# Kernel tuning notes

Measured on AMD Instinct MI355X. Metric: run time of the kernel, lower is better.

## Reference

```python
import jax, jax.numpy as jnp
import numpy as np

N = 100000     # nodes
E = 1600000    # edges (avg degree 16)
CI = 3         # input features (x, z, t)
W = 128        # hidden width
CO = 1         # output features
L = 4          # processor layers


def setup_inputs() -> dict:
    key = jax.random.key(0)
    ks = jax.random.split(key, 10)
    s = 0.1
    x = jax.random.normal(ks[0], (N, CI), jnp.float32)
    # compute_mask is an external geometry-dependent, no-grad mask; emulate as 0/1 node mask
    mask = (jax.random.uniform(ks[1], (N, 1)) > 0.5).astype(jnp.float32)
    edge_index = jax.random.randint(ks[2], (2, E), 0, N, dtype=jnp.int32)
    W_enc = jax.random.normal(ks[3], (CI, W), jnp.float32) * s
    b_enc = jnp.zeros((W,), jnp.float32)
    W_p = jax.random.normal(ks[4], (L, W, W), jnp.float32) * s
    b_p = jnp.zeros((L, W), jnp.float32)
    W_dec = jax.random.normal(ks[5], (W, CO), jnp.float32) * s
    b_dec = jnp.zeros((CO,), jnp.float32)
    return {"x": x, "mask": mask, "edge_index": edge_index,
            "W_enc": W_enc, "b_enc": b_enc, "W_p": W_p, "b_p": b_p,
            "W_dec": W_dec, "b_dec": b_dec}


def reference(x, mask, edge_index, W_enc, b_enc, W_p, b_p, W_dec, b_dec):
    src, dst = edge_index[0], edge_index[1]
    n = x.shape[0]
    # GCN symmetric normalization with self-loops: deg = 1 + in-degree
    deg = 1.0 + jax.ops.segment_sum(jnp.ones((src.shape[0],), x.dtype), dst, num_segments=n)
    dis = jax.lax.rsqrt(deg)                      # deg^{-1/2}, [N]
    norm = dis[src] * dis[dst]                    # [E]

    def gcn(h, Wt, b):
        h = h @ Wt                                # [N, out]
        agg = jax.ops.segment_sum(h[src] * norm[:, None], dst, num_segments=n)
        # self-loop contribution: norm_ii = dis_i^2
        return agg + h * (dis * dis)[:, None] + b

    h = jax.nn.relu(gcn(x, W_enc, b_enc))
    for l in range(L):
        h = jax.nn.relu(gcn(h, W_p[l], b_p[l]))
    out = gcn(h, W_dec, b_dec)
    return out * mask
```

## Files before the change

### kernel.cpp

```cpp
#include <hip/hip_runtime.h>
#include <hip/hip_fp16.h>


#define HW 128
#define NBMAX 1024
#define CAP 4096
#define PBLK 256

typedef _Float16 f16x8 __attribute__((ext_vector_type(8)));
typedef float f32x4 __attribute__((ext_vector_type(4)));

__global__ void k_zero_i32(int* __restrict__ a, int n) {
    int i = blockIdx.x * 256 + threadIdx.x;
    if (i < n) a[i] = 0;
}

__global__ __launch_bounds__(256) void k_histb(const int* __restrict__ dstA,
                                               int* __restrict__ bcnt,
                                               int* __restrict__ pcnt,
                                               int nb, int e, int nblk) {
    __shared__ int lh[NBMAX];
    for (int b = threadIdx.x; b < nb; b += 256) lh[b] = 0;
    __syncthreads();
    int blk = blockIdx.x;
    int c0 = (int)(((long long)e * blk) / nblk);
    int c1 = (int)(((long long)e * (blk + 1)) / nblk);
    for (int i = c0 + threadIdx.x; i < c1; i += 256) atomicAdd(&lh[dstA[i] >> 7], 1);
    __syncthreads();
    for (int b = threadIdx.x; b < nb; b += 256) {
        int v = lh[b];
        pcnt[(size_t)blk * nb + b] = v;
        if (v) atomicAdd(&bcnt[b], v);
    }
}

__global__ void k_bscan(const int* __restrict__ bcnt, int* __restrict__ bstart,
                        int nb, int etot) {
    __shared__ int s[1024];
    int t = threadIdx.x;
    int d0 = (t < nb) ? bcnt[t] : 0;
    s[t] = d0;
    __syncthreads();
    for (int off = 1; off < 1024; off <<= 1) {
        int v = (t >= off) ? s[t - off] : 0;
        __syncthreads();
        s[t] += v;
        __syncthreads();
    }
    if (t < nb) bstart[t] = s[t] - d0;
    if (t == 0) bstart[nb] = etot;
}

__global__ __launch_bounds__(PBLK) void k_soff2(const int* __restrict__ pcnt,
                                                const int* __restrict__ bstart,
                                                int* __restrict__ soff, int nb) {
    __shared__ int s[PBLK];
    int b = blockIdx.x, t = threadIdx.x;
    int v = pcnt[(size_t)t * nb + b];
    s[t] = v;
    __syncthreads();
    for (int off = 1; off < PBLK; off <<= 1) {
        int u = (t >= off) ? s[t - off] : 0;
        __syncthreads();
        s[t] += u;
        __syncthreads();
    }
    soff[(size_t)t * nb + b] = bstart[b] + s[t] - v;
}

__global__ __launch_bounds__(256) void k_part(const int* __restrict__ srcA,
                                              const int* __restrict__ dstA,
                                              const int* __restrict__ soff,
                                              unsigned* __restrict__ stage,
                                              int nb, int e, int nblk) {
    __shared__ int loff[NBMAX];
    __shared__ int lh[NBMAX];
    int blk = blockIdx.x;
    for (int b = threadIdx.x; b < nb; b += 256) {
        loff[b] = soff[(size_t)blk * nb + b];
        lh[b] = 0;
    }
    __syncthreads();
    int c0 = (int)(((long long)e * blk) / nblk);
    int c1 = (int)(((long long)e * (blk + 1)) / nblk);
    for (int i = c0 + threadIdx.x; i < c1; i += 256) {
        int d = dstA[i];
        int bk = d >> 7;
        int p = loff[bk] + atomicAdd(&lh[bk], 1);
        stage[p] = ((unsigned)srcA[i] << 7) | (unsigned)(d & 127);
    }
}

__global__ __launch_bounds__(256) void k_build(const unsigned* __restrict__ stage,
                                               const int* __restrict__ bstart,
                                               const float* __restrict__ x,
                                               int* __restrict__ row_start,
                                               float* __restrict__ dis,
                                               float4* __restrict__ x4,
                                               int* __restrict__ csr, int n, int nb) {
    __shared__ int lcnt[128];
    __shared__ int sc[128];
    __shared__ int lcsr[CAP];
    int b = blockIdx.x, tid = threadIdx.x;
    int base = bstart[b], end = bstart[b + 1], cnt = end - base;
    int node0 = b << 7;

    if (tid < 128) lcnt[tid] = 0;
    __syncthreads();
    for (int j = tid; j < cnt; j += 256) atomicAdd(&lcnt[stage[base + j] & 127], 1);
    __syncthreads();
    if (tid < 128) sc[tid] = lcnt[tid];
    __syncthreads();
    for (int off = 1; off < 128; off <<= 1) {
        int v = (tid < 128 && tid >= off) ? sc[tid - off] : 0;
        __syncthreads();
        if (tid < 128) sc[tid] += v;
        __syncthreads();
    }
    int node = node0 + tid;
    if (tid < 128 && node < n) {
        int excl = sc[tid] - lcnt[tid];
        row_start[node] = base + excl;
        float dv = rsqrtf(1.f + (float)lcnt[tid]);
        dis[node] = dv;
        x4[node] = make_float4(x[node * 3] * dv, x[node * 3 + 1] * dv,
                               x[node * 3 + 2] * dv, 0.f);
    }
    if (tid == 0 && b == nb - 1) row_start[n] = end;
    __syncthreads();
    if (tid < 128) sc[tid] = sc[tid] - lcnt[tid];
    if (tid < 128) lcnt[tid] = 0;
    __syncthreads();
    if (cnt <= CAP) {
        for (int j = tid; j < cnt; j += 256) {
            unsigned v = stage[base + j];
            int dl = v & 127;
            int p = atomicAdd(&lcnt[dl], 1);
            lcsr[sc[dl] + p] = (int)(v >> 7);
        }
        __syncthreads();
        for (int j = tid; j < cnt; j += 256) csr[base + j] = lcsr[j];
    } else {
        for (int j = tid; j < cnt; j += 256) {
            unsigned v = stage[base + j];
            int dl = v & 127;
            int p = atomicAdd(&lcnt[dl], 1);
            csr[base + sc[dl] + p] = (int)(v >> 7);
        }
    }
}

__global__ void k_prep_wt(const float* __restrict__ Wp, __half* __restrict__ WTh,
                          __half* __restrict__ WTl, int total) {
    int t = blockIdx.x * 256 + threadIdx.x;
    if (t >= total) return;
    int l = t >> 14;
    int kc = t & 16383;
    int k = kc >> 7, c = kc & 127;
    float w = Wp[t];
    __half hi = __float2half_rn(w);
    __half lo = __float2half_rn(w - __half2float(hi));
    size_t o = ((size_t)l << 14) + (size_t)c * HW + k;
    WTh[o] = hi;
    WTl[o] = lo;
}

__global__ void k_enc_agg(const float4* __restrict__ x4, const int* __restrict__ rs,
                          const int* __restrict__ csr, const float* __restrict__ dis,
                          float4* __restrict__ zx, int n) {
    int i = blockIdx.x * 256 + threadIdx.x;
    if (i >= n) return;
    float4 a = x4[i];
    int e1 = rs[i + 1];
    for (int j = rs[i]; j < e1; ++j) {
        float4 v = x4[csr[j]];
        a.x += v.x; a.y += v.y; a.z += v.z;
    }
    float d = dis[i];
    zx[i] = make_float4(a.x * d, a.y * d, a.z * d, 0.f);
}

__global__ void k_enc_gemm(const float4* __restrict__ zx, const float* __restrict__ We,
                           const float* __restrict__ be, const float* __restrict__ dis,
                           __half* __restrict__ H, int n) {
    int t = blockIdx.x * 256 + threadIdx.x;
    int i = t >> 7;
    int c = t & 127;
    if (i >= n) return;
    float4 z = zx[i];
    float v = z.x * We[c] + z.y * We[HW + c] + z.z * We[2 * HW + c] + be[c];
    H[(size_t)i * HW + c] = __float2half_rn(fmaxf(v, 0.f) * dis[i]);
}

__global__ __launch_bounds__(256) void k_agg128(const __half* __restrict__ Hin,
                                                const int* __restrict__ rs,
                                                const int* __restrict__ csr,
                                                const float* __restrict__ dis,
                                                __half* __restrict__ Z, int n) {
    int wave = threadIdx.x >> 6, lane = threadIdx.x & 63;
    int lg = lane & 15;
    int node = (blockIdx.x * 4 + wave) * 4 + (lane >> 4);
    bool active = node < n;

    float a0[8], a1[8], a2[8], a3[8];
#pragma unroll
    for (int j = 0; j < 8; ++j) { a0[j] = 0.f; a1[j] = 0.f; a2[j] = 0.f; a3[j] = 0.f; }

    int e0 = 0, e1 = 0;
    if (active) {
        e0 = rs[node];
        e1 = rs[node + 1];
        f16x8 hv = *(const f16x8*)(Hin + (size_t)node * HW + lg * 8);
#pragma unroll
        for (int j = 0; j < 8; ++j) a0[j] = (float)hv[j];
    }

    for (int base = e0; base < e1; base += 16) {
        int cnt = e1 - base;
        if (cnt > 16) cnt = 16;
        int sl = (base + lg < e1) ? csr[base + lg] : 0;
        int k = 0;
        for (; k + 4 <= cnt; k += 4) {
            int s0 = __shfl(sl, k + 0, 16);
            int s1 = __shfl(sl, k + 1, 16);
            int s2 = __shfl(sl, k + 2, 16);
            int s3 = __shfl(sl, k + 3, 16);
            f16x8 v0 = *(const f16x8*)(Hin + (size_t)s0 * HW + lg * 8);
            f16x8 v1 = *(const f16x8*)(Hin + (size_t)s1 * HW + lg * 8);
            f16x8 v2 = *(const f16x8*)(Hin + (size_t)s2 * HW + lg * 8);
            f16x8 v3 = *(const f16x8*)(Hin + (size_t)s3 * HW + lg * 8);
#pragma unroll
            for (int j = 0; j < 8; ++j) {
                a0[j] += (float)v0[j];
                a1[j] += (float)v1[j];
                a2[j] += (float)v2[j];
                a3[j] += (float)v3[j];
            }
        }
        for (; k < cnt; ++k) {
            int s = __shfl(sl, k, 16);
            f16x8 v = *(const f16x8*)(Hin + (size_t)s * HW + lg * 8);
#pragma unroll
            for (int j = 0; j < 8; ++j) a0[j] += (float)v[j];
        }
    }

    if (active) {
        float d = dis[node];
        union { uint4 u; __half2 h[4]; } pk;
#pragma unroll
        for (int j = 0; j < 4; ++j) {
            float lo = d * ((a0[2 * j] + a1[2 * j]) + (a2[2 * j] + a3[2 * j]));
            float hi = d * ((a0[2 * j + 1] + a1[2 * j + 1]) + (a2[2 * j + 1] + a3[2 * j + 1]));
            pk.h[j] = __floats2half2_rn(lo, hi);
        }
        *(uint4*)(Z + (size_t)node * HW + lg * 8) = pk.u;
    }
}

#define GBM 256
__global__ __launch_bounds__(256) void k_gemm_mfma(const __half* __restrict__ Z,
                                                   const __half* __restrict__ WTh,
                                                   const __half* __restrict__ WTl,
                                                   const float* __restrict__ b,
                                                   const float* __restrict__ dis,
                                                   __half* __restrict__ Hout,
                                                   const float* __restrict__ Wd,
                                                   float* __restrict__ tout,
                                                   int mode, int n) {
    int wave = threadIdx.x >> 6, lane = threadIdx.x & 63;
    int q = lane >> 4, r16 = lane & 15;
    int row0 = blockIdx.x * GBM + wave * 64;

    f32x4 acc[4][8];
#pragma unroll
    for (int mt = 0; mt < 4; ++mt)
#pragma unroll
        for (int nt = 0; nt < 8; ++nt) acc[mt][nt] = (f32x4)0.f;

#pragma unroll
    for (int ks = 0; ks < 4; ++ks) {
        f16x8 afr[4];
#pragma unroll
        for (int mt = 0; mt < 4; ++mt) {
            int row = row0 + mt * 16 + r16;
            row = row < n ? row : (n - 1);
            afr[mt] = *(const f16x8*)(Z + (size_t)row * HW + ks * 32 + q * 8);
        }
#pragma unroll
        for (int nt = 0; nt < 8; ++nt) {
            f16x8 bh = *(const f16x8*)(WTh + (size_t)(nt * 16 + r16) * HW + ks * 32 + q * 8);
            f16x8 bl = *(const f16x8*)(WTl + (size_t)(nt * 16 + r16) * HW + ks * 32 + q * 8);
#pragma unroll
            for (int mt = 0; mt < 4; ++mt) {
                acc[mt][nt] = __builtin_amdgcn_mfma_f32_16x16x32_f16(afr[mt], bh, acc[mt][nt], 0, 0, 0);
                acc[mt][nt] = __builtin_amdgcn_mfma_f32_16x16x32_f16(afr[mt], bl, acc[mt][nt], 0, 0, 0);
            }
        }
    }

    float dr[4][4];
#pragma unroll
    for (int mt = 0; mt < 4; ++mt)
#pragma unroll
        for (int r = 0; r < 4; ++r) {
            int row = row0 + mt * 16 + q * 4 + r;
            dr[mt][r] = (row < n) ? dis[row] : 0.f;
        }
    float bias[8];
#pragma unroll
    for (int nt = 0; nt < 8; ++nt) bias[nt] = b[nt * 16 + r16];

    if (mode == 0) {
#pragma unroll
        for (int nt = 0; nt < 8; ++nt) {
#pragma unroll
            for (int mt = 0; mt < 4; ++mt) {
#pragma unroll
                for (int r = 0; r < 4; ++r) {
                    int row = row0 + mt * 16 + q * 4 + r;
                    if (row < n) {
                        float v = fmaxf(acc[mt][nt][r] + bias[nt], 0.f) * dr[mt][r];
                        Hout[(size_t)row * HW + nt * 16 + r16] = __float2half_rn(v);
                    }
                }
            }
        }
    } else {
        float wd[8];
#pragma unroll
        for (int nt = 0; nt < 8; ++nt) wd[nt] = Wd[nt * 16 + r16];
#pragma unroll
        for (int mt = 0; mt < 4; ++mt) {
#pragma unroll
            for (int r = 0; r < 4; ++r) {
                float pr = 0.f;
#pragma unroll
                for (int nt = 0; nt < 8; ++nt)
                    pr += fmaxf(acc[mt][nt][r] + bias[nt], 0.f) * wd[nt];
                pr *= dr[mt][r];
#pragma unroll
                for (int off = 1; off < 16; off <<= 1) pr += __shfl_xor(pr, off, 16);
                if (r16 == 0) {
                    int row = row0 + mt * 16 + q * 4 + r;
                    if (row < n) tout[row] = pr;
                }
            }
        }
    }
}

__global__ void k_dec_out(const float* __restrict__ t, const int* __restrict__ rs,
                          const int* __restrict__ csr, const float* __restrict__ dis,
                          const float* __restrict__ bdec, const float* __restrict__ mask,
                          float* __restrict__ out, int n) {
    int i = blockIdx.x * 256 + threadIdx.x;
    if (i >= n) return;
    float acc = t[i];
    int e1 = rs[i + 1];
    for (int j = rs[i]; j < e1; ++j) acc += t[csr[j]];
    out[i] = (dis[i] * acc + bdec[0]) * mask[i];
}

static inline size_t align256(size_t x) { return (x + 255) & ~(size_t)255; }

extern "C" void kernel_launch(void* const* d_in, const int* in_sizes, int n_in,
                              void* d_out, int out_size, void* d_ws, size_t ws_size,
                              hipStream_t stream) {
    const float* x     = (const float*)d_in[0];
    const float* mask  = (const float*)d_in[1];
    const int*   ei    = (const int*)d_in[2];
    const float* W_enc = (const float*)d_in[3];
    const float* b_enc = (const float*)d_in[4];
    const float* W_p   = (const float*)d_in[5];
    const float* b_p   = (const float*)d_in[6];
    const float* W_dec = (const float*)d_in[7];
    const float* b_dec = (const float*)d_in[8];

    const int N = in_sizes[1];
    const int E = in_sizes[2] / 2;
    const int* srcA = ei;
    const int* dstA = ei + E;
    const int NB = (N + 127) >> 7;

    char* p = (char*)d_ws;
    size_t off = 0;
    auto carve = [&](size_t bytes) {
        void* r = p + off;
        off += align256(bytes);
        return r;
    };
    int*      bcnt      = (int*)carve((size_t)NB * 4);
    int*      bstart    = (int*)carve((size_t)(NB + 1) * 4);
    int*      pcnt      = (int*)carve((size_t)PBLK * NB * 4);
    int*      soff      = (int*)carve((size_t)PBLK * NB * 4);
    int*      row_start = (int*)carve((size_t)(N + 1) * 4);
    unsigned* stage     = (unsigned*)carve((size_t)E * 4);
    int*      csr       = (int*)carve((size_t)E * 4);
    float*    dis       = (float*)carve((size_t)N * 4);
    float4*   x4        = (float4*)carve((size_t)N * 16);
    float4*   zx        = (float4*)carve((size_t)N * 16);
    float*    tdec      = (float*)carve((size_t)N * 4);
    __half*   WTh       = (__half*)carve((size_t)4 * HW * HW * 2);
    __half*   WTl       = (__half*)carve((size_t)4 * HW * HW * 2);
    __half*   HA        = (__half*)carve((size_t)N * HW * 2);
    __half*   HB        = (__half*)carve((size_t)N * HW * 2);

    const int gN   = (N + 255) / 256;
    const int gAgg = (N + 15) / 16;
    const int gG   = (N + GBM - 1) / GBM;
    const int WPT  = 4 * HW * HW;

    k_zero_i32<<<(NB + 255) / 256, 256, 0, stream>>>(bcnt, NB);
    k_histb<<<PBLK, 256, 0, stream>>>(dstA, bcnt, pcnt, NB, E, PBLK);
    k_bscan<<<1, 1024, 0, stream>>>(bcnt, bstart, NB, E);
    k_soff2<<<NB, PBLK, 0, stream>>>(pcnt, bstart, soff, NB);
    k_part<<<PBLK, 256, 0, stream>>>(srcA, dstA, soff, stage, NB, E, PBLK);
    k_build<<<NB, 256, 0, stream>>>(stage, bstart, x, row_start, dis, x4, csr, N, NB);
    k_prep_wt<<<(WPT + 255) / 256, 256, 0, stream>>>(W_p, WTh, WTl, WPT);

    k_enc_agg<<<gN, 256, 0, stream>>>(x4, row_start, csr, dis, zx, N);
    k_enc_gemm<<<(N * HW + 255) / 256, 256, 0, stream>>>(zx, W_enc, b_enc, dis, HA, N);

    __half* Hin = HA;
    __half* Hoth = HB;
    for (int l = 0; l < 4; ++l) {
        k_agg128<<<gAgg, 256, 0, stream>>>(Hin, row_start, csr, dis, Hoth, N);
        int mode = (l == 3) ? 1 : 0;
        k_gemm_mfma<<<gG, 256, 0, stream>>>(Hoth, WTh + (size_t)l * HW * HW,
                                            WTl + (size_t)l * HW * HW,
                                            b_p + (size_t)l * HW, dis, Hoth,
                                            W_dec, tdec, mode, N);
        __half* t = Hin; Hin = Hoth; Hoth = t;
    }

    k_dec_out<<<gN, 256, 0, stream>>>(tdec, row_start, csr, dis, b_dec, mask,
                                      (float*)d_out, N);
}
```

Before: 513.2 us.

## Fuse neighbor aggregation and MFMA GEMM into one per-layer kernel

Merges the gather-aggregation kernel and the MFMA GEMM kernel into a single per-layer kernel. Each 16-node block aggregates its rows into LDS, then each of the four waves computes a 32-column slice of the 16x128 output. This drops the Z intermediate round trip through global memory and one launch per layer. In exchange every block re-reads the full split-fp16 weight matrices, GEMM tiles are much smaller with less weight reuse, and the decoder path needs an extra cross-wave LDS reduction.

```diff
diff --git a/kernel.cpp b/kernel.cpp
--- a/kernel.cpp
+++ b/kernel.cpp
@@ -192,14 +192,23 @@
     H[(size_t)i * HW + c] = __float2half_rn(fmaxf(v, 0.f) * dis[i]);
 }
 
-__global__ __launch_bounds__(256) void k_agg128(const __half* __restrict__ Hin,
-                                                const int* __restrict__ rs,
-                                                const int* __restrict__ csr,
-                                                const float* __restrict__ dis,
-                                                __half* __restrict__ Z, int n) {
+__global__ __launch_bounds__(256) void k_layer(const __half* __restrict__ Hin,
+                                               const int* __restrict__ rs,
+                                               const int* __restrict__ csr,
+                                               const float* __restrict__ dis,
+                                               const __half* __restrict__ WTh,
+                                               const __half* __restrict__ WTl,
+                                               const float* __restrict__ b,
+                                               __half* __restrict__ Hout,
+                                               const float* __restrict__ Wd,
+                                               float* __restrict__ tout,
+                                               int mode, int n) {
+    __shared__ __half zs[16][136];
+    __shared__ float psum[4][16];
     int wave = threadIdx.x >> 6, lane = threadIdx.x & 63;
     int lg = lane & 15;
-    int node = (blockIdx.x * 4 + wave) * 4 + (lane >> 4);
+    int ln = wave * 4 + (lane >> 4);
+    int node = blockIdx.x * 16 + ln;
     bool active = node < n;
 
     float a0[8], a1[8], a2[8], a3[8];
@@ -245,8 +254,8 @@
         }
     }
 
-    if (active) {
-        float d = dis[node];
+    {
+        float d = active ? dis[node] : 0.f;
         union { uint4 u; __half2 h[4]; } pk;
 #pragma unroll
         for (int j = 0; j < 4; ++j) {
@@ -254,97 +263,68 @@
             float hi = d * ((a0[2 * j + 1] + a1[2 * j + 1]) + (a2[2 * j + 1] + a3[2 * j + 1]));
             pk.h[j] = __floats2half2_rn(lo, hi);
         }
-        *(uint4*)(Z + (size_t)node * HW + lg * 8) = pk.u;
-    }
-}
-
-#define GBM 256
-__global__ __launch_bounds__(256) void k_gemm_mfma(const __half* __restrict__ Z,
-                                                   const __half* __restrict__ WTh,
-                                                   const __half* __restrict__ WTl,
-                                                   const float* __restrict__ b,
-                                                   const float* __restrict__ dis,
-                                                   __half* __restrict__ Hout,
-                                                   const float* __restrict__ Wd,
-                                                   float* __restrict__ tout,
-                                                   int mode, int n) {
-    int wave = threadIdx.x >> 6, lane = threadIdx.x & 63;
+        *(uint4*)&zs[ln][lg * 8] = pk.u;
+    }
+    __syncthreads();
+
     int q = lane >> 4, r16 = lane & 15;
-    int row0 = blockIdx.x * GBM + wave * 64;
-
-    f32x4 acc[4][8];
-#pragma unroll
-    for (int mt = 0; mt < 4; ++mt)
-#pragma unroll
-        for (int nt = 0; nt < 8; ++nt) acc[mt][nt] = (f32x4)0.f;
-
+    f32x4 acc[2];
+    acc[0] = (f32x4)0.f;
+    acc[1] = (f32x4)0.f;
 #pragma unroll
     for (int ks = 0; ks < 4; ++ks) {
-        f16x8 afr[4];
-#pragma unroll
-        for (int mt = 0; mt < 4; ++mt) {
-            int row = row0 + mt * 16 + r16;
-            row = row < n ? row : (n - 1);
-            afr[mt] = *(const f16x8*)(Z + (size_t)row * HW + ks * 32 + q * 8);
-        }
-#pragma unroll
-        for (int nt = 0; nt < 8; ++nt) {
-            f16x8 bh = *(const f16x8*)(WTh + (size_t)(nt * 16 + r16) * HW + ks * 32 + q * 8);
-            f16x8 bl = *(const f16x8*)(WTl + (size_t)(nt * 16 + r16) * HW + ks * 32 + q * 8);
-#pragma unroll
-            for (int mt = 0; mt < 4; ++mt) {
-                acc[mt][nt] = __builtin_amdgcn_mfma_f32_16x16x32_f16(afr[mt], bh, acc[mt][nt], 0, 0, 0);
-                acc[mt][nt] = __builtin_amdgcn_mfma_f32_16x16x32_f16(afr[mt], bl, acc[mt][nt], 0, 0, 0);
-            }
-        }
-    }
-
-    float dr[4][4];
-#pragma unroll
-    for (int mt = 0; mt < 4; ++mt)
-#pragma unroll
-        for (int r = 0; r < 4; ++r) {
-            int row = row0 + mt * 16 + q * 4 + r;
-            dr[mt][r] = (row < n) ? dis[row] : 0.f;
-        }
-    float bias[8];
-#pragma unroll
-    for (int nt = 0; nt < 8; ++nt) bias[nt] = b[nt * 16 + r16];
-
+        f16x8 afr = *(const f16x8*)&zs[r16][ks * 32 + q * 8];
+#pragma unroll
+        for (int ntl = 0; ntl < 2; ++ntl) {
+            int col = wave * 32 + ntl * 16 + r16;
+            f16x8 bh = *(const f16x8*)(WTh + (size_t)col * HW + ks * 32 + q * 8);
+            f16x8 bl = *(const f16x8*)(WTl + (size_t)col * HW + ks * 32 + q * 8);
+            acc[ntl] = __builtin_amdgcn_mfma_f32_16x16x32_f16(afr, bh, acc[ntl], 0, 0, 0);
+            acc[ntl] = __builtin_amdgcn_mfma_f32_16x16x32_f16(afr, bl, acc[ntl], 0, 0, 0);
+        }
+    }
+
+    int row0 = blockIdx.x * 16;
     if (mode == 0) {
 #pragma unroll
-        for (int nt = 0; nt < 8; ++nt) {
-#pragma unroll
-            for (int mt = 0; mt < 4; ++mt) {
-#pragma unroll
-                for (int r = 0; r < 4; ++r) {
-                    int row = row0 + mt * 16 + q * 4 + r;
-                    if (row < n) {
-                        float v = fmaxf(acc[mt][nt][r] + bias[nt], 0.f) * dr[mt][r];
-                        Hout[(size_t)row * HW + nt * 16 + r16] = __float2half_rn(v);
-                    }
+        for (int ntl = 0; ntl < 2; ++ntl) {
+            int col = wave * 32 + ntl * 16 + r16;
+            float bias = b[col];
+#pragma unroll
+            for (int r = 0; r < 4; ++r) {
+                int row = row0 + q * 4 + r;
+                if (row < n) {
+                    float v = fmaxf(acc[ntl][r] + bias, 0.f) * dis[row];
+                    Hout[(size_t)row * HW + col] = __float2half_rn(v);
                 }
             }
         }
     } else {
-        float wd[8];
-#pragma unroll
-        for (int nt = 0; nt < 8; ++nt) wd[nt] = Wd[nt * 16 + r16];
-#pragma unroll
-        for (int mt = 0; mt < 4; ++mt) {
-#pragma unroll
-            for (int r = 0; r < 4; ++r) {
-                float pr = 0.f;
-#pragma unroll
-                for (int nt = 0; nt < 8; ++nt)
-                    pr += fmaxf(acc[mt][nt][r] + bias[nt], 0.f) * wd[nt];
-                pr *= dr[mt][r];
-#pragma unroll
-                for (int off = 1; off < 16; off <<= 1) pr += __shfl_xor(pr, off, 16);
-                if (r16 == 0) {
-                    int row = row0 + mt * 16 + q * 4 + r;
-                    if (row < n) tout[row] = pr;
-                }
+        float pr[4];
+#pragma unroll
+        for (int r = 0; r < 4; ++r) pr[r] = 0.f;
+#pragma unroll
+        for (int ntl = 0; ntl < 2; ++ntl) {
+            int col = wave * 32 + ntl * 16 + r16;
+            float bias = b[col];
+            float wd = Wd[col];
+#pragma unroll
+            for (int r = 0; r < 4; ++r)
+                pr[r] += fmaxf(acc[ntl][r] + bias, 0.f) * wd;
+        }
+#pragma unroll
+        for (int r = 0; r < 4; ++r) {
+#pragma unroll
+            for (int off = 1; off < 16; off <<= 1) pr[r] += __shfl_xor(pr[r], off, 16);
+            if (r16 == 0) psum[wave][q * 4 + r] = pr[r];
+        }
+        __syncthreads();
+        if (threadIdx.x < 16) {
+            int row = row0 + threadIdx.x;
+            if (row < n) {
+                float t = (psum[0][threadIdx.x] + psum[1][threadIdx.x]) +
+                          (psum[2][threadIdx.x] + psum[3][threadIdx.x]);
+                tout[row] = t * dis[row];
             }
         }
     }
@@ -407,8 +387,7 @@
     __half*   HB        = (__half*)carve((size_t)N * HW * 2);
 
     const int gN   = (N + 255) / 256;
-    const int gAgg = (N + 15) / 16;
-    const int gG   = (N + GBM - 1) / GBM;
+    const int gL   = (N + 15) / 16;
     const int WPT  = 4 * HW * HW;
 
     k_zero_i32<<<(NB + 255) / 256, 256, 0, stream>>>(bcnt, NB);
@@ -423,15 +402,15 @@
     k_enc_gemm<<<(N * HW + 255) / 256, 256, 0, stream>>>(zx, W_enc, b_enc, dis, HA, N);
 
     __half* Hin = HA;
-    __half* Hoth = HB;
+    __half* Hout = HB;
     for (int l = 0; l < 4; ++l) {
-        k_agg128<<<gAgg, 256, 0, stream>>>(Hin, row_start, csr, dis, Hoth, N);
         int mode = (l == 3) ? 1 : 0;
-        k_gemm_mfma<<<gG, 256, 0, stream>>>(Hoth, WTh + (size_t)l * HW * HW,
-                                            WTl + (size_t)l * HW * HW,
-                                            b_p + (size_t)l * HW, dis, Hoth,
-                                            W_dec, tdec, mode, N);
-        __half* t = Hin; Hin = Hoth; Hoth = t;
+        k_layer<<<gL, 256, 0, stream>>>(Hin, row_start, csr, dis,
+                                        WTh + (size_t)l * HW * HW,
+                                        WTl + (size_t)l * HW * HW,
+                                        b_p + (size_t)l * HW, Hout,
+                                        W_dec, tdec, mode, N);
+        __half* t = Hin; Hin = Hout; Hout = t;
     }
 
     k_dec_out<<<gN, 256, 0, stream>>>(tdec, row_start, csr, dis, b_dec, mask,
```

Result: no change. 506.8 us (-1.3%).
